# Kernel optimization log

Measured on AMD Instinct MI355X. Metric: run time of the kernel, lower is better.

## Reference

```python
import jax, jax.numpy as jnp
import numpy as np

N = 100000        # nodes
E = 3200000       # edges (before self loops)
DIN = 128         # dim_input
DOUT = 64         # dim_output
HID = 4           # per-head hidden of conv1
HEADS = 8         # num_in_head
G = 64            # number of graphs in the batch
NEG_SLOPE = 0.2   # PyG GATConv default


def _gat_conv(x, edge_index, W, att_src, att_dst, bias, concat):
    """PyG GATConv (add_self_loops=True, dropout inactive / eval mode)."""
    n = x.shape[0]
    heads, dout = att_src.shape
    h = (x @ W).reshape(n, heads, dout)                  # [N, H, F]
    loop = jnp.arange(n)
    src = jnp.concatenate([edge_index[0], loop])          # [Et]
    dst = jnp.concatenate([edge_index[1], loop])          # [Et]
    a_s = (h * att_src).sum(-1)                           # [N, H]
    a_d = (h * att_dst).sum(-1)                           # [N, H]
    alpha = jax.nn.leaky_relu(a_s[src] + a_d[dst], NEG_SLOPE)   # [Et, H]
    amax = jax.ops.segment_max(alpha, dst, num_segments=n)      # softmax over in-edges
    ex = jnp.exp(alpha - amax[dst])
    denom = jax.ops.segment_sum(ex, dst, num_segments=n)
    w = ex / (denom[dst] + 1e-16)                         # [Et, H]
    out = jax.ops.segment_sum(h[src] * w[:, :, None], dst, num_segments=n)  # [N, H, F]
    out = out.reshape(n, heads * dout) if concat else out.mean(axis=1)
    return out + bias


def setup_inputs() -> dict:
    key = jax.random.key(0)
    ks = jax.random.split(key, 11)
    x = jax.random.normal(ks[0], (N, DIN), jnp.float32)
    edge_index = jax.random.randint(ks[1], (2, E), 0, N)
    batch = jnp.sort(jax.random.randint(ks[2], (N,), 0, G))
    s1 = 1.0 / np.sqrt(DIN)
    W1 = jax.random.uniform(ks[3], (DIN, HEADS * HID), jnp.float32, -s1, s1)
    att_src1 = jax.random.normal(ks[4], (HEADS, HID), jnp.float32) * 0.1
    att_dst1 = jax.random.normal(ks[5], (HEADS, HID), jnp.float32) * 0.1
    b1 = jnp.zeros((HEADS * HID,), jnp.float32)
    s2 = 1.0 / np.sqrt(HEADS * HID)
    W2 = jax.random.uniform(ks[6], (HEADS * HID, DOUT), jnp.float32, -s2, s2)
    att_src2 = jax.random.normal(ks[7], (1, DOUT), jnp.float32) * 0.1
    att_dst2 = jax.random.normal(ks[8], (1, DOUT), jnp.float32) * 0.1
    b2 = jnp.zeros((DOUT,), jnp.float32)
    return {"x": x, "edge_index": edge_index, "batch": batch,
            "W1": W1, "att_src1": att_src1, "att_dst1": att_dst1, "b1": b1,
            "W2": W2, "att_src2": att_src2, "att_dst2": att_dst2, "b2": b2}


def reference(x, edge_index, batch, W1, att_src1, att_dst1, b1,
              W2, att_src2, att_dst2, b2):
    h = _gat_conv(x, edge_index, W1, att_src1, att_dst1, b1, concat=True)
    h = jax.nn.elu(h)
    h = _gat_conv(h, edge_index, W2, att_src2, att_dst2, b2, concat=False)
    # global_mean_pool over batch ids
    sums = jax.ops.segment_sum(h, batch, num_segments=G)          # [G, DOUT]
    counts = jax.ops.segment_sum(jnp.ones((N,), h.dtype), batch, num_segments=G)
    return sums / jnp.maximum(counts, 1.0)[:, None]
```

## Files before the change

kernel.cpp:

```cpp
#include <hip/hip_runtime.h>
#include <math.h>

static constexpr int NN   = 100000;
static constexpr int NE   = 3200000;
static constexpr int ET   = NE + NN;
static constexpr int DIN  = 128;
static constexpr int H1   = 8;
static constexpr int C1   = 32;
static constexpr int DOUT = 64;
static constexpr int NG   = 64;
static constexpr int NB_SCAN = (NN + 255) / 256;
static constexpr int SLAB = (NN + 255) / 256;

__device__ __forceinline__ float lrelu(float x){ return x > 0.f ? x : 0.2f*x; }
__device__ __forceinline__ float bfl(unsigned int u){ return __uint_as_float(u << 16); }
__device__ __forceinline__ float bfh(unsigned int u){ return __uint_as_float(u & 0xffff0000u); }
__device__ __forceinline__ unsigned short f2bf(float x){
  unsigned int u = __float_as_uint(x);
  u += 0x7fffu + ((u >> 16) & 1u);
  return (unsigned short)(u >> 16);
}

__global__ __launch_bounds__(256) void k_gemm1(const float* __restrict__ x,
                                               const float* __restrict__ W,
                                               const float* __restrict__ as1,
                                               const float* __restrict__ ad1,
                                               unsigned short* __restrict__ h1b,
                                               float* __restrict__ a_s,
                                               float* __restrict__ a_d){
  __shared__ float w[DIN * C1];
  for (int i = threadIdx.x; i < DIN * C1; i += 256) w[i] = W[i];
  __syncthreads();
  int idx = blockIdx.x * 256 + threadIdx.x;
  int n = idx >> 5, j = idx & 31;
  const float* xr = x + (size_t)n * DIN;
  float acc = 0.f;
  #pragma unroll
  for (int k = 0; k < DIN; ++k) acc += xr[k] * w[k * C1 + j];
  h1b[idx] = f2bf(acc);
  float s = acc * as1[j], d = acc * ad1[j];
  s += __shfl_xor(s, 1, 64); s += __shfl_xor(s, 2, 64);
  d += __shfl_xor(d, 1, 64); d += __shfl_xor(d, 2, 64);
  if ((j & 3) == 0){ a_s[n * H1 + (j >> 2)] = s; a_d[n * H1 + (j >> 2)] = d; }
}

__global__ __launch_bounds__(256) void k_init_cnt(int* __restrict__ cnt){
  int n = blockIdx.x * 256 + threadIdx.x;
  if (n < NN) cnt[n] = 1;
}

__global__ __launch_bounds__(256) void k_hist(const int* __restrict__ ei, int* __restrict__ cnt){
  int e = blockIdx.x * 256 + threadIdx.x;
  atomicAdd(&cnt[ei[NE + e]], 1);
}

__global__ __launch_bounds__(256) void k_scan_blk(const int* __restrict__ cnt,
                                                  int* __restrict__ tmp, int* __restrict__ btot){
  int g = blockIdx.x * 256 + threadIdx.x;
  int v = (g < NN) ? cnt[g] : 0;
  int lane = threadIdx.x & 63, wv = threadIdx.x >> 6;
  int xv = v;
  #pragma unroll
  for (int o = 1; o < 64; o <<= 1){ int y = __shfl_up(xv, o, 64); if (lane >= o) xv += y; }
  __shared__ int ws[4];
  if (lane == 63) ws[wv] = xv;
  __syncthreads();
  int off = 0;
  for (int i = 0; i < wv; ++i) off += ws[i];
  xv += off;
  if (g < NN) tmp[g] = xv;
  if (threadIdx.x == 255) btot[blockIdx.x] = xv;
}

__global__ __launch_bounds__(512) void k_scan_top(int* __restrict__ btot){
  int t = threadIdx.x;
  int v = (t < NB_SCAN) ? btot[t] : 0;
  int lane = t & 63, wv = t >> 6;
  int xv = v;
  #pragma unroll
  for (int o = 1; o < 64; o <<= 1){ int y = __shfl_up(xv, o, 64); if (lane >= o) xv += y; }
  __shared__ int ws[8];
  if (lane == 63) ws[wv] = xv;
  __syncthreads();
  int off = 0;
  for (int i = 0; i < wv; ++i) off += ws[i];
  xv += off;
  if (t < NB_SCAN) btot[t] = xv - v;
}

__global__ __launch_bounds__(256) void k_scan_fin(const int* __restrict__ cnt,
                                                  const int* __restrict__ tmp,
                                                  const int* __restrict__ btot,
                                                  int* __restrict__ row, int* __restrict__ cur){
  int g = blockIdx.x * 256 + threadIdx.x;
  if (g < NN){
    int ex = tmp[g] - cnt[g] + btot[g >> 8];
    row[g] = ex; cur[g] = ex;
  } else if (g == NN){
    row[NN] = ET;
  }
}

__global__ __launch_bounds__(256) void k_scatter(const int* __restrict__ ei,
                                                 int* __restrict__ cur, int* __restrict__ ssrc){
  int e = blockIdx.x * 256 + threadIdx.x;
  if (e >= ET) return;
  int s, d;
  if (e < NE) { s = ei[e]; d = ei[NE + e]; }
  else        { s = e - NE; d = s; }
  int pos = atomicAdd(&cur[d], 1);
  ssrc[pos] = s;
}

__global__ __launch_bounds__(256, 4) void k_agg1(const int* __restrict__ row,
                                              const int* __restrict__ ssrc,
                                              const float* __restrict__ a_s,
                                              const float* __restrict__ a_d,
                                              const unsigned short* __restrict__ h1b,
                                              const float* __restrict__ b1,
                                              float* __restrict__ out1){
  int node = (blockIdx.x * 256 + threadIdx.x) >> 6;
  int lane = threadIdx.x & 63;
  int l = lane & 7, g = lane >> 3;
  float adv = a_d[node * H1 + l];
  int beg = row[node], end = row[node + 1];
  float a0 = 0.f, a1 = 0.f, a2 = 0.f, a3 = 0.f, den = 0.f;
  for (int base = beg; base < end; base += 64){
    int sv[8]; float liv[8];
    #pragma unroll
    for (int u = 0; u < 8; ++u){
      int k = base + u * 8 + g;
      liv[u] = (k < end) ? 1.f : 0.f;
      sv[u] = ssrc[k < end ? k : end - 1];
    }
    uint2 hraw[8]; float araw[8];
    #pragma unroll
    for (int u = 0; u < 8; ++u){
      hraw[u] = *(const uint2*)(h1b + (size_t)sv[u] * C1 + 4 * l);
      araw[u] = a_s[sv[u] * H1 + l];
    }
    #pragma unroll
    for (int u = 0; u < 8; ++u){
      float al = liv[u] * __expf(lrelu(araw[u] + adv));
      den += al;
      a0 += al * bfl(hraw[u].x); a1 += al * bfh(hraw[u].x);
      a2 += al * bfl(hraw[u].y); a3 += al * bfh(hraw[u].y);
    }
  }
  #pragma unroll
  for (int o = 8; o < 64; o <<= 1){
    den += __shfl_xor(den, o, 64);
    a0 += __shfl_xor(a0, o, 64); a1 += __shfl_xor(a1, o, 64);
    a2 += __shfl_xor(a2, o, 64); a3 += __shfl_xor(a3, o, 64);
  }
  if (g == 0){
    float r = 1.f / den;
    float4 bv = *(const float4*)(b1 + 4 * l);
    float v0 = a0 * r + bv.x, v1 = a1 * r + bv.y, v2 = a2 * r + bv.z, v3 = a3 * r + bv.w;
    v0 = v0 > 0.f ? v0 : expm1f(v0); v1 = v1 > 0.f ? v1 : expm1f(v1);
    v2 = v2 > 0.f ? v2 : expm1f(v2); v3 = v3 > 0.f ? v3 : expm1f(v3);
    *(float4*)(out1 + (size_t)node * C1 + 4 * l) = make_float4(v0, v1, v2, v3);
  }
}

__global__ __launch_bounds__(256) void k_gemm2(const float* __restrict__ hin,
                                               const float* __restrict__ W,
                                               const float* __restrict__ as2,
                                               const float* __restrict__ ad2,
                                               unsigned short* __restrict__ h2b,
                                               float* __restrict__ a_s,
                                               float* __restrict__ a_d){
  __shared__ float w[C1 * DOUT];
  for (int i = threadIdx.x; i < C1 * DOUT; i += 256) w[i] = W[i];
  __syncthreads();
  int idx = blockIdx.x * 256 + threadIdx.x;
  int n = idx >> 6, j = idx & 63;
  const float* hr = hin + (size_t)n * C1;
  float acc = 0.f;
  #pragma unroll
  for (int k = 0; k < C1; ++k) acc += hr[k] * w[k * DOUT + j];
  h2b[idx] = f2bf(acc);
  float s = acc * as2[j], d = acc * ad2[j];
  #pragma unroll
  for (int o = 1; o < 64; o <<= 1){ s += __shfl_xor(s, o, 64); d += __shfl_xor(d, o, 64); }
  if (j == 0){ a_s[n] = s; a_d[n] = d; }
}

__global__ __launch_bounds__(256, 4) void k_agg2(const int* __restrict__ row,
                                              const int* __restrict__ ssrc,
                                              const float* __restrict__ a_s,
                                              const float* __restrict__ a_d,
                                              const unsigned short* __restrict__ h2b,
                                              float* __restrict__ out2){
  int node = (blockIdx.x * 256 + threadIdx.x) >> 6;
  int lane = threadIdx.x & 63;
  int l = lane & 15, g = lane >> 4;
  float adv = a_d[node];
  int beg = row[node], end = row[node + 1];
  float ac0 = 0.f, ac1 = 0.f, ac2 = 0.f, ac3 = 0.f, den = 0.f;
  for (int base = beg; base < end; base += 32){
    int sv[8]; float liv[8];
    #pragma unroll
    for (int u = 0; u < 8; ++u){
      int k = base + u * 4 + g;
      liv[u] = (k < end) ? 1.f : 0.f;
      sv[u] = ssrc[k < end ? k : end - 1];
    }
    uint2 hraw[8]; float asv[8];
    #pragma unroll
    for (int u = 0; u < 8; ++u){
      hraw[u] = *(const uint2*)(h2b + (size_t)sv[u] * DOUT + 4 * l);
      asv[u] = a_s[sv[u]];
    }
    #pragma unroll
    for (int u = 0; u < 8; ++u){
      float al = liv[u] * __expf(lrelu(asv[u] + adv));
      den += al;
      ac0 += al * bfl(hraw[u].x); ac1 += al * bfh(hraw[u].x);
      ac2 += al * bfl(hraw[u].y); ac3 += al * bfh(hraw[u].y);
    }
  }
  #pragma unroll
  for (int o = 16; o < 64; o <<= 1){
    den += __shfl_xor(den, o, 64);
    ac0 += __shfl_xor(ac0, o, 64); ac1 += __shfl_xor(ac1, o, 64);
    ac2 += __shfl_xor(ac2, o, 64); ac3 += __shfl_xor(ac3, o, 64);
  }
  if (g == 0){
    float r = 1.f / den;
    *(float4*)(out2 + (size_t)node * DOUT + 4 * l) =
        make_float4(ac0 * r, ac1 * r, ac2 * r, ac3 * r);
  }
}

__global__ __launch_bounds__(256) void k_bounds(const int* __restrict__ batch,
                                                int* __restrict__ gs){
  int n = blockIdx.x * 256 + threadIdx.x;
  if (n >= NN) return;
  int b = batch[n];
  if (n == 0) gs[b] = 0;
  else if (batch[n - 1] != b) gs[b] = n;
}

__global__ void k_fix(int* __restrict__ gs){
  if (threadIdx.x == 0){
    gs[NG] = NN;
    for (int g = NG - 1; g >= 0; --g) if (gs[g] < 0) gs[g] = gs[g + 1];
  }
}

__global__ __launch_bounds__(256) void k_pool(const float* __restrict__ out2,
                                              const int* __restrict__ batch,
                                              float* __restrict__ sums){
  int start = blockIdx.x * SLAB;
  int stop  = start + SLAB; if (stop > NN) stop = NN;
  int wv = threadIdx.x >> 6, lane = threadIdx.x & 63;
  int n0 = start + wv;
  if (n0 >= stop) return;
  float acc = 0.f;
  int cur_g = batch[n0];
  for (int n = n0; n < stop; n += 4){
    int g = batch[n];
    if (g != cur_g){
      atomicAdd(&sums[cur_g * DOUT + lane], acc);
      acc = 0.f; cur_g = g;
    }
    acc += out2[(size_t)n * DOUT + lane];
  }
  atomicAdd(&sums[cur_g * DOUT + lane], acc);
}

__global__ __launch_bounds__(256) void k_final(const float* __restrict__ sums,
                                               const int* __restrict__ gs,
                                               const float* __restrict__ b2,
                                               float* __restrict__ out){
  int idx = blockIdx.x * 256 + threadIdx.x;
  if (idx >= NG * DOUT) return;
  int g = idx >> 6, f = idx & 63;
  int c = gs[g + 1] - gs[g];
  out[idx] = sums[idx] / (float)(c > 0 ? c : 1) + b2[f];
}

extern "C" void kernel_launch(void* const* d_in, const int* in_sizes, int n_in,
                              void* d_out, int out_size, void* d_ws, size_t ws_size,
                              hipStream_t stream) {
  const float* x   = (const float*)d_in[0];
  const int*   ei  = (const int*)  d_in[1];
  const int*   bat = (const int*)  d_in[2];
  const float* W1  = (const float*)d_in[3];
  const float* as1 = (const float*)d_in[4];
  const float* ad1 = (const float*)d_in[5];
  const float* b1  = (const float*)d_in[6];
  const float* W2  = (const float*)d_in[7];
  const float* as2 = (const float*)d_in[8];
  const float* ad2 = (const float*)d_in[9];
  const float* b2  = (const float*)d_in[10];
  float* out = (float*)d_out;

  char* p = (char*)d_ws;
  auto alloc = [&](size_t bytes){ void* r = p; p += (bytes + 255) & ~(size_t)255; return r; };
  unsigned short* h1b  = (unsigned short*)alloc((size_t)NN * C1 * 2);
  float* a_s1  = (float*)alloc((size_t)NN * H1 * 4);
  float* a_d1  = (float*)alloc((size_t)NN * H1 * 4);
  float* out1  = (float*)alloc((size_t)NN * C1 * 4);
  unsigned short* h2b  = (unsigned short*)alloc((size_t)NN * DOUT * 2);
  float* a_s2  = (float*)alloc(NN * 4);
  float* a_d2  = (float*)alloc(NN * 4);
  float* out2  = (float*)alloc((size_t)NN * DOUT * 4);
  int*   row   = (int*)alloc((NN + 1) * 4);
  int*   cur   = (int*)alloc(NN * 4);
  int*   tmp   = (int*)alloc(NN * 4);
  int*   btot  = (int*)alloc(512 * 4);
  int*   cnt   = (int*)alloc(NN * 4);
  int*   ssrc  = (int*)alloc((size_t)ET * 4);
  float* sums  = (float*)alloc(NG * DOUT * 4);
  int*   gs    = (int*)alloc((NG + 1) * 4);

  hipMemsetAsync(sums, 0, NG * DOUT * 4, stream);
  hipMemsetAsync(gs, 0xFF, (NG + 1) * 4, stream);
  k_init_cnt<<<(NN + 255) / 256, 256, 0, stream>>>(cnt);

  k_gemm1<<<(NN * C1) / 256, 256, 0, stream>>>(x, W1, as1, ad1, h1b, a_s1, a_d1);

  k_hist    <<<NE / 256, 256, 0, stream>>>(ei, cnt);
  k_scan_blk<<<NB_SCAN, 256, 0, stream>>>(cnt, tmp, btot);
  k_scan_top<<<1, 512, 0, stream>>>(btot);
  k_scan_fin<<<(NN + 256) / 256, 256, 0, stream>>>(cnt, tmp, btot, row, cur);
  k_scatter <<<(ET + 255) / 256, 256, 0, stream>>>(ei, cur, ssrc);

  k_bounds<<<(NN + 255) / 256, 256, 0, stream>>>(bat, gs);
  k_fix<<<1, 64, 0, stream>>>(gs);

  k_agg1<<<(NN * 64) / 256, 256, 0, stream>>>(row, ssrc, a_s1, a_d1, h1b, b1, out1);

  k_gemm2<<<(NN * DOUT) / 256, 256, 0, stream>>>(out1, W2, as2, ad2, h2b, a_s2, a_d2);
  k_agg2 <<<(NN * 64) / 256, 256, 0, stream>>>(row, ssrc, a_s2, a_d2, h2b, out2);

  k_pool <<<256, 256, 0, stream>>>(out2, bat, sums);
  k_final<<<(NG * DOUT + 255) / 256, 256, 0, stream>>>(sums, gs, b2, out);
}
```

Measured before the change: 762.6 us.

## Build CSR via two-level bucket partition with shared-memory local sort

Replaces the per-node global histogram, three-pass scan and per-node atomic scatter with a coarse partition into 64-node buckets, followed by a per-bucket shared-memory counting sort that writes row offsets and sorted sources. This targets the cost of 3.3M global atomics spread across 100k counters and the scattered writes that come with them. In exchange it adds an intermediate int2 edge-pair buffer, an extra pass over the edges, and a serial single-wavefront scan over roughly 1.5k buckets. The coarse atomics now land on far fewer addresses, so contention on those counters may rise.

```diff
diff --git a/kernel.cpp b/kernel.cpp
--- a/kernel.cpp
+++ b/kernel.cpp
@@ -9,7 +9,8 @@
 static constexpr int C1   = 32;
 static constexpr int DOUT = 64;
 static constexpr int NG   = 64;
-static constexpr int NB_SCAN = (NN + 255) / 256;
+static constexpr int BSZ  = 64;
+static constexpr int NB   = (NN + BSZ - 1) / BSZ;
 static constexpr int SLAB = (NN + 255) / 256;
 
 __device__ __forceinline__ float lrelu(float x){ return x > 0.f ? x : 0.2f*x; }
@@ -44,72 +45,75 @@
   if ((j & 3) == 0){ a_s[n * H1 + (j >> 2)] = s; a_d[n * H1 + (j >> 2)] = d; }
 }
 
-__global__ __launch_bounds__(256) void k_init_cnt(int* __restrict__ cnt){
-  int n = blockIdx.x * 256 + threadIdx.x;
-  if (n < NN) cnt[n] = 1;
-}
-
-__global__ __launch_bounds__(256) void k_hist(const int* __restrict__ ei, int* __restrict__ cnt){
+__global__ __launch_bounds__(256) void k_binit(int* __restrict__ bcnt){
+  int b = blockIdx.x * 256 + threadIdx.x;
+  if (b < NB){
+    int rem = NN - b * BSZ;
+    bcnt[b] = rem < BSZ ? rem : BSZ;
+  }
+}
+
+__global__ __launch_bounds__(256) void k_bhist(const int* __restrict__ ei, int* __restrict__ bcnt){
   int e = blockIdx.x * 256 + threadIdx.x;
-  atomicAdd(&cnt[ei[NE + e]], 1);
-}
-
-__global__ __launch_bounds__(256) void k_scan_blk(const int* __restrict__ cnt,
-                                                  int* __restrict__ tmp, int* __restrict__ btot){
-  int g = blockIdx.x * 256 + threadIdx.x;
-  int v = (g < NN) ? cnt[g] : 0;
-  int lane = threadIdx.x & 63, wv = threadIdx.x >> 6;
-  int xv = v;
-  #pragma unroll
-  for (int o = 1; o < 64; o <<= 1){ int y = __shfl_up(xv, o, 64); if (lane >= o) xv += y; }
-  __shared__ int ws[4];
-  if (lane == 63) ws[wv] = xv;
-  __syncthreads();
-  int off = 0;
-  for (int i = 0; i < wv; ++i) off += ws[i];
-  xv += off;
-  if (g < NN) tmp[g] = xv;
-  if (threadIdx.x == 255) btot[blockIdx.x] = xv;
-}
-
-__global__ __launch_bounds__(512) void k_scan_top(int* __restrict__ btot){
-  int t = threadIdx.x;
-  int v = (t < NB_SCAN) ? btot[t] : 0;
-  int lane = t & 63, wv = t >> 6;
-  int xv = v;
-  #pragma unroll
-  for (int o = 1; o < 64; o <<= 1){ int y = __shfl_up(xv, o, 64); if (lane >= o) xv += y; }
-  __shared__ int ws[8];
-  if (lane == 63) ws[wv] = xv;
-  __syncthreads();
-  int off = 0;
-  for (int i = 0; i < wv; ++i) off += ws[i];
-  xv += off;
-  if (t < NB_SCAN) btot[t] = xv - v;
-}
-
-__global__ __launch_bounds__(256) void k_scan_fin(const int* __restrict__ cnt,
-                                                  const int* __restrict__ tmp,
-                                                  const int* __restrict__ btot,
-                                                  int* __restrict__ row, int* __restrict__ cur){
-  int g = blockIdx.x * 256 + threadIdx.x;
-  if (g < NN){
-    int ex = tmp[g] - cnt[g] + btot[g >> 8];
-    row[g] = ex; cur[g] = ex;
-  } else if (g == NN){
-    row[NN] = ET;
-  }
-}
-
-__global__ __launch_bounds__(256) void k_scatter(const int* __restrict__ ei,
-                                                 int* __restrict__ cur, int* __restrict__ ssrc){
+  atomicAdd(&bcnt[ei[NE + e] >> 6], 1);
+}
+
+__global__ __launch_bounds__(64) void k_bscan(const int* __restrict__ bcnt,
+                                              int* __restrict__ bbase, int* __restrict__ bcur,
+                                              int* __restrict__ row){
+  int lane = threadIdx.x;
+  int running = 0;
+  for (int c = 0; c < (NB + 63) / 64; ++c){
+    int i = c * 64 + lane;
+    int v = (i < NB) ? bcnt[i] : 0;
+    int xv = v;
+    #pragma unroll
+    for (int o = 1; o < 64; o <<= 1){ int y = __shfl_up(xv, o, 64); if (lane >= o) xv += y; }
+    int ex = running + xv - v;
+    if (i < NB){ bbase[i] = ex; bcur[i] = ex; }
+    running = __shfl(running + xv, 63, 64);
+  }
+  if (lane == 0){ bbase[NB] = ET; row[NN] = ET; }
+}
+
+__global__ __launch_bounds__(256) void k_bpart(const int* __restrict__ ei,
+                                               int* __restrict__ bcur, int2* __restrict__ epair){
   int e = blockIdx.x * 256 + threadIdx.x;
   if (e >= ET) return;
   int s, d;
   if (e < NE) { s = ei[e]; d = ei[NE + e]; }
   else        { s = e - NE; d = s; }
-  int pos = atomicAdd(&cur[d], 1);
-  ssrc[pos] = s;
+  int pos = atomicAdd(&bcur[d >> 6], 1);
+  epair[pos] = make_int2(s, d);
+}
+
+__global__ __launch_bounds__(256) void k_bsort(const int* __restrict__ bbase,
+                                               const int2* __restrict__ epair,
+                                               int* __restrict__ row, int* __restrict__ ssrc){
+  __shared__ int lcnt[BSZ];
+  int b = blockIdx.x, tid = threadIdx.x;
+  int node0 = b * BSZ;
+  int beg = bbase[b], end = bbase[b + 1];
+  if (tid < BSZ) lcnt[tid] = 0;
+  __syncthreads();
+  for (int i = beg + tid; i < end; i += 256)
+    atomicAdd(&lcnt[epair[i].y - node0], 1);
+  __syncthreads();
+  if (tid < BSZ){
+    int v = lcnt[tid];
+    int xv = v;
+    #pragma unroll
+    for (int o = 1; o < 64; o <<= 1){ int y = __shfl_up(xv, o, 64); if (tid >= o) xv += y; }
+    int ex = beg + xv - v;
+    if (node0 + tid < NN) row[node0 + tid] = ex;
+    lcnt[tid] = ex;
+  }
+  __syncthreads();
+  for (int i = beg + tid; i < end; i += 256){
+    int2 sd = epair[i];
+    int pos = atomicAdd(&lcnt[sd.y - node0], 1);
+    ssrc[pos] = sd.x;
+  }
 }
 
 __global__ __launch_bounds__(256, 4) void k_agg1(const int* __restrict__ row,
@@ -308,25 +312,24 @@
   float* a_d2  = (float*)alloc(NN * 4);
   float* out2  = (float*)alloc((size_t)NN * DOUT * 4);
   int*   row   = (int*)alloc((NN + 1) * 4);
-  int*   cur   = (int*)alloc(NN * 4);
-  int*   tmp   = (int*)alloc(NN * 4);
-  int*   btot  = (int*)alloc(512 * 4);
-  int*   cnt   = (int*)alloc(NN * 4);
+  int*   bcnt  = (int*)alloc((NB + 1) * 4);
+  int*   bbase = (int*)alloc((NB + 1) * 4);
+  int*   bcur  = (int*)alloc(NB * 4);
+  int2*  epair = (int2*)alloc((size_t)ET * 8);
   int*   ssrc  = (int*)alloc((size_t)ET * 4);
   float* sums  = (float*)alloc(NG * DOUT * 4);
   int*   gs    = (int*)alloc((NG + 1) * 4);
 
   hipMemsetAsync(sums, 0, NG * DOUT * 4, stream);
   hipMemsetAsync(gs, 0xFF, (NG + 1) * 4, stream);
-  k_init_cnt<<<(NN + 255) / 256, 256, 0, stream>>>(cnt);
 
   k_gemm1<<<(NN * C1) / 256, 256, 0, stream>>>(x, W1, as1, ad1, h1b, a_s1, a_d1);
 
-  k_hist    <<<NE / 256, 256, 0, stream>>>(ei, cnt);
-  k_scan_blk<<<NB_SCAN, 256, 0, stream>>>(cnt, tmp, btot);
-  k_scan_top<<<1, 512, 0, stream>>>(btot);
-  k_scan_fin<<<(NN + 256) / 256, 256, 0, stream>>>(cnt, tmp, btot, row, cur);
-  k_scatter <<<(ET + 255) / 256, 256, 0, stream>>>(ei, cur, ssrc);
+  k_binit<<<(NB + 255) / 256, 256, 0, stream>>>(bcnt);
+  k_bhist<<<NE / 256, 256, 0, stream>>>(ei, bcnt);
+  k_bscan<<<1, 64, 0, stream>>>(bcnt, bbase, bcur, row);
+  k_bpart<<<(ET + 255) / 256, 256, 0, stream>>>(ei, bcur, epair);
+  k_bsort<<<NB, 256, 0, stream>>>(bbase, epair, row, ssrc);
 
   k_bounds<<<(NN + 255) / 256, 256, 0, stream>>>(bat, gs);
   k_fix<<<1, 64, 0, stream>>>(gs);
```

New measurement: 1.416 ms. 1.86x slower.
